# Kernel tuning notes

Hardware: AMD Instinct MI355X
Metric: run time of the kernel (lower is better)

Reference implementation:

```python
import jax, jax.numpy as jnp
import numpy as np

B, S, K, N = 4, 2048, 4096, 4096

def setup_inputs() -> dict:
    key = jax.random.key(0)
    k1, k2, k3, k4 = jax.random.split(key, 4)
    # int8 quantized activations and weight (stored as int8, matmul accumulates int32)
    a = jax.random.randint(k1, (B, S, K), -128, 128, dtype=jnp.int32).astype(jnp.int8)
    w = jax.random.randint(k3, (K, N), -128, 128, dtype=jnp.int32).astype(jnp.int8)
    # dequant scales: per-token for activations, per-output-channel for weight
    a_s = (jax.random.uniform(k2, (B, S, 1), dtype=jnp.float32) + 0.5) * 0.01
    w_s = (jax.random.uniform(k4, (1, N), dtype=jnp.float32) + 0.5) * 0.01
    return {"a": a, "a_s": a_s, "w": w, "w_s": w_s}

def reference(a, a_s, w, w_s):
    # torch._int_mm loop with padding), fused with dequant epilogue.
    acc = jnp.einsum('bsk,kn->bsn', a, w, preferred_element_type=jnp.int32)
    # dequant: float32 accum * input_scale * weight_scale, cast to model dtype (fp16)
    out = (acc.astype(jnp.float32) * a_s * w_s).astype(jnp.float16)
    return out
```

## Files before the change

### kernel.cpp

```cpp
#include <hip/hip_runtime.h>
#include <cstdint>
#include <cstddef>


#define M_DIM 8192
#define N_DIM 4096
#define K_DIM 4096

#define PACKA_BLOCKS ((M_DIM * K_DIM / 4) / 256)
#define TRANS_BLOCKS ((N_DIM / 64) * (K_DIM / 64))

typedef int v4i  __attribute__((ext_vector_type(4)));
typedef int v16i __attribute__((ext_vector_type(16)));

__device__ __forceinline__ uint32_t pack4(int x, int y, int z, int w)
{
    return (uint32_t)(x & 0xff) | ((uint32_t)(y & 0xff) << 8) |
           ((uint32_t)(z & 0xff) << 16) | ((uint32_t)(w & 0xff) << 24);
}

__global__ void __launch_bounds__(256) prepare_kernel(
    const int* __restrict__ a, const int* __restrict__ w,
    uint8_t* __restrict__ pa, uint8_t* __restrict__ wt)
{
    __shared__ int lds[64][65];

    if (blockIdx.x < PACKA_BLOCKS) {
        const size_t idx = (size_t)blockIdx.x * 256 + threadIdx.x;
        int4 x = ((const int4*)a)[idx];
        ((uint32_t*)pa)[idx] = pack4(x.x, x.y, x.z, x.w);
        return;
    }

    const int tile = blockIdx.x - PACKA_BLOCKS;
    const int t  = threadIdx.x;
    const int n0 = (tile & 63) * 64;
    const int k0 = (tile >> 6) * 64;

#pragma unroll
    for (int i = 0; i < 4; ++i) {
        int v   = t + 256 * i;
        int row = v >> 4;
        int cq  = v & 15;
        int4 x = *(const int4*)(w + (size_t)(k0 + row) * N_DIM + n0 + cq * 4);
        lds[row][cq * 4 + 0] = x.x;
        lds[row][cq * 4 + 1] = x.y;
        lds[row][cq * 4 + 2] = x.z;
        lds[row][cq * 4 + 3] = x.w;
    }
    __syncthreads();

    const int n_local = t >> 2;
    const int c       = t & 3;
    uint32_t o[4];
#pragma unroll
    for (int j = 0; j < 4; ++j)
        o[j] = pack4(lds[c * 16 + j * 4 + 0][n_local],
                     lds[c * 16 + j * 4 + 1][n_local],
                     lds[c * 16 + j * 4 + 2][n_local],
                     lds[c * 16 + j * 4 + 3][n_local]);
    *(uint4*)(wt + (size_t)(n0 + n_local) * K_DIM + k0 + c * 16) =
        make_uint4(o[0], o[1], o[2], o[3]);
}

__device__ __forceinline__ void async_copy16(const void* gptr, void* lptr)
{
    __builtin_amdgcn_global_load_lds(
        (const __attribute__((address_space(1))) uint32_t*)gptr,
        (__attribute__((address_space(3))) uint32_t*)lptr,
        16, 0, 0);
}

#define VMCNT4() asm volatile("s_waitcnt vmcnt(4)" ::: "memory")
#define VMCNT0() asm volatile("s_waitcnt vmcnt(0)" ::: "memory")

__global__ void __launch_bounds__(512, 2) int8_gemm_kernel(
    const uint8_t* __restrict__ A,
    const uint8_t* __restrict__ Wt,
    const float*   __restrict__ a_s,
    const float*   __restrict__ w_s,
    float*         __restrict__ out)
{
    __shared__ __align__(16) uint8_t sA[2][2][256 * 64];
    __shared__ __align__(16) uint8_t sB[2][2][256 * 64];

    const int tid   = threadIdx.x;
    const int wave  = tid >> 6;
    const int lane  = tid & 63;
    const int waveM = wave >> 2;
    const int waveN = wave & 3;

    const int bm = blockIdx.x & 31;
    const int bn = blockIdx.x >> 5;
    const int m0 = bm * 256;
    const int n0 = bn * 256;

    v16i acc[4][2];
#pragma unroll
    for (int i = 0; i < 4; ++i)
#pragma unroll
        for (int j = 0; j < 2; ++j)
#pragma unroll
            for (int r = 0; r < 16; ++r)
                acc[i][j][r] = 0;

    auto stageA = [&](int buf, int kh, int kt) {
#pragma unroll
        for (int l = 0; l < 2; ++l) {
            const int region = l * 8 + wave;
            const int i      = region * 64 + lane;
            const int row    = i >> 2;
            const int g      = (i & 3) ^ ((row >> 1) & 3);
            async_copy16(A + (size_t)(m0 + row) * K_DIM + kt * 128 + kh * 64 + g * 16,
                         &sA[buf][kh][region * 1024]);
        }
    };
    auto stageB = [&](int buf, int kh, int kt) {
#pragma unroll
        for (int l = 0; l < 2; ++l) {
            const int region = l * 8 + wave;
            const int i      = region * 64 + lane;
            const int row    = i >> 2;
            const int g      = (i & 3) ^ ((row >> 1) & 3);
            async_copy16(Wt + (size_t)(n0 + row) * K_DIM + kt * 128 + kh * 64 + g * 16,
                         &sB[buf][kh][region * 1024]);
        }
    };

    const int frow = lane & 31;
    const int fk   = lane >> 5;

    auto compute_kstep = [&](int buf, int s) {
        const int kh = s >> 1;
        const int c  = (s & 1) * 2 + fk;
        v4i af[4], bf[2];
#pragma unroll
        for (int mt = 0; mt < 4; ++mt) {
            const int ra = waveM * 128 + mt * 32 + frow;
            af[mt] = *(const v4i*)(&sA[buf][kh][ra * 64 + ((c ^ ((ra >> 1) & 3)) << 4)]);
        }
#pragma unroll
        for (int nt = 0; nt < 2; ++nt) {
            const int rb = waveN * 64 + nt * 32 + frow;
            bf[nt] = *(const v4i*)(&sB[buf][kh][rb * 64 + ((c ^ ((rb >> 1) & 3)) << 4)]);
        }
        __builtin_amdgcn_s_setprio(1);
#pragma unroll
        for (int mt = 0; mt < 4; ++mt)
#pragma unroll
            for (int nt = 0; nt < 2; ++nt)
                acc[mt][nt] = __builtin_amdgcn_mfma_i32_32x32x32_i8(
                    af[mt], bf[nt], acc[mt][nt], 0, 0, 0);
        __builtin_amdgcn_s_setprio(0);
    };

    const int NT = K_DIM / 128;

    stageA(0, 0, 0);
    stageB(0, 0, 0);
    stageA(0, 1, 0);
    stageB(0, 1, 0);
    VMCNT4();
    __builtin_amdgcn_s_barrier();

    for (int kt = 0; kt < NT - 1; ++kt) {
        const int b = kt & 1;
        stageA(b ^ 1, 0, kt + 1);
        compute_kstep(b, 0);
        stageB(b ^ 1, 0, kt + 1);
        compute_kstep(b, 1);
        VMCNT4();
        __builtin_amdgcn_s_barrier();
        stageA(b ^ 1, 1, kt + 1);
        compute_kstep(b, 2);
        stageB(b ^ 1, 1, kt + 1);
        compute_kstep(b, 3);
        VMCNT4();
        __builtin_amdgcn_s_barrier();
    }
    {
        const int b = (NT - 1) & 1;
        compute_kstep(b, 0);
        compute_kstep(b, 1);
        VMCNT0();
        __builtin_amdgcn_s_barrier();
        compute_kstep(b, 2);
        compute_kstep(b, 3);
    }

    const int col   = lane & 31;
    const int rbase = (lane >> 5) * 4;

#pragma unroll
    for (int mt = 0; mt < 4; ++mt) {
        const int mrow0 = m0 + waveM * 128 + mt * 32 + rbase;
        float asv[16];
#pragma unroll
        for (int reg = 0; reg < 16; ++reg)
            asv[reg] = a_s[mrow0 + (reg & 3) + 8 * (reg >> 2)];
#pragma unroll
        for (int nt = 0; nt < 2; ++nt) {
            const int n = n0 + waveN * 64 + nt * 32 + col;
            const float wsv = w_s[n];
#pragma unroll
            for (int reg = 0; reg < 16; ++reg) {
                const int row = mrow0 + (reg & 3) + 8 * (reg >> 2);
                float v = (float)acc[mt][nt][reg] * asv[reg] * wsv;
                v = (float)(_Float16)v;
                out[(size_t)row * N_DIM + n] = v;
            }
        }
    }
}

extern "C" void kernel_launch(void* const* d_in, const int* in_sizes, int n_in,
                              void* d_out, int out_size, void* d_ws, size_t ws_size,
                              hipStream_t stream)
{
    const int*   a   = (const int*)  d_in[0];
    const float* a_s = (const float*)d_in[1];
    const int*   w   = (const int*)  d_in[2];
    const float* w_s = (const float*)d_in[3];
    float*       out = (float*)d_out;

    uint8_t* wt = (uint8_t*)d_ws;
    uint8_t* pa = (uint8_t*)d_ws + (size_t)N_DIM * K_DIM;

    prepare_kernel<<<PACKA_BLOCKS + TRANS_BLOCKS, 256, 0, stream>>>(a, w, pa, wt);

    int8_gemm_kernel<<<(M_DIM / 256) * (N_DIM / 256), 512, 0, stream>>>(
        pa, wt, a_s, w_s, out);
}
```

Measured before the change: 422.3 us.

## Store LDS tiles in MFMA fragment order, simplify pipeline, remap blocks per XCD

Reorganizes shared memory so each async global-to-LDS copy lands a 32-row by 32-byte block in exact MFMA operand order. Fragment reads become linear lane*16 loads with no XOR swizzle arithmetic. The pipeline is simplified to one full-tile prefetch per iteration with a single vmcnt(0) wait and barrier, which removes the finer split overlap. Blocks are also remapped so consecutive IDs on each XCD cover 8x8 tile neighborhoods, aiming at better L2 reuse, at the risk of coarser synchronization stalls.

```diff
diff --git a/kernel.cpp b/kernel.cpp
--- a/kernel.cpp
+++ b/kernel.cpp
@@ -71,7 +71,6 @@
         16, 0, 0);
 }
 
-#define VMCNT4() asm volatile("s_waitcnt vmcnt(4)" ::: "memory")
 #define VMCNT0() asm volatile("s_waitcnt vmcnt(0)" ::: "memory")
 
 __global__ void __launch_bounds__(512, 2) int8_gemm_kernel(
@@ -81,8 +80,8 @@
     const float*   __restrict__ w_s,
     float*         __restrict__ out)
 {
-    __shared__ __align__(16) uint8_t sA[2][2][256 * 64];
-    __shared__ __align__(16) uint8_t sB[2][2][256 * 64];
+    __shared__ __align__(16) uint8_t sA[2][4][8][1024];
+    __shared__ __align__(16) uint8_t sB[2][4][8][1024];
 
     const int tid   = threadIdx.x;
     const int wave  = tid >> 6;
@@ -90,60 +89,45 @@
     const int waveM = wave >> 2;
     const int waveN = wave & 3;
 
-    const int bm = blockIdx.x & 31;
-    const int bn = blockIdx.x >> 5;
-    const int m0 = bm * 256;
-    const int n0 = bn * 256;
+    const int bid = blockIdx.x;
+    const int xc  = bid & 7;
+    const int j   = bid >> 3;
+    const int bm  = (xc & 3) * 8 + (j & 7);
+    const int bn  = (xc >> 2) * 8 + (j >> 3);
+    const int m0  = bm * 256;
+    const int n0  = bn * 256;
 
     v16i acc[4][2];
 #pragma unroll
     for (int i = 0; i < 4; ++i)
 #pragma unroll
-        for (int j = 0; j < 2; ++j)
+        for (int jj = 0; jj < 2; ++jj)
 #pragma unroll
             for (int r = 0; r < 16; ++r)
-                acc[i][j][r] = 0;
-
-    auto stageA = [&](int buf, int kh, int kt) {
-#pragma unroll
-        for (int l = 0; l < 2; ++l) {
-            const int region = l * 8 + wave;
-            const int i      = region * 64 + lane;
-            const int row    = i >> 2;
-            const int g      = (i & 3) ^ ((row >> 1) & 3);
-            async_copy16(A + (size_t)(m0 + row) * K_DIM + kt * 128 + kh * 64 + g * 16,
-                         &sA[buf][kh][region * 1024]);
+                acc[i][jj][r] = 0;
+
+    const uint8_t* aSrc = A  + (size_t)(m0 + wave * 32 + (lane & 31)) * K_DIM
+                             + ((lane >> 5) << 4);
+    const uint8_t* bSrc = Wt + (size_t)(n0 + wave * 32 + (lane & 31)) * K_DIM
+                             + ((lane >> 5) << 4);
+
+    auto stage_tile = [&](int buf, int kt) {
+        const int ko = kt * 128;
+#pragma unroll
+        for (int s = 0; s < 4; ++s) {
+            async_copy16(aSrc + ko + s * 32, &sA[buf][s][wave][0]);
+            async_copy16(bSrc + ko + s * 32, &sB[buf][s][wave][0]);
         }
     };
-    auto stageB = [&](int buf, int kh, int kt) {
-#pragma unroll
-        for (int l = 0; l < 2; ++l) {
-            const int region = l * 8 + wave;
-            const int i      = region * 64 + lane;
-            const int row    = i >> 2;
-            const int g      = (i & 3) ^ ((row >> 1) & 3);
-            async_copy16(Wt + (size_t)(n0 + row) * K_DIM + kt * 128 + kh * 64 + g * 16,
-                         &sB[buf][kh][region * 1024]);
-        }
-    };
-
-    const int frow = lane & 31;
-    const int fk   = lane >> 5;
 
     auto compute_kstep = [&](int buf, int s) {
-        const int kh = s >> 1;
-        const int c  = (s & 1) * 2 + fk;
         v4i af[4], bf[2];
 #pragma unroll
-        for (int mt = 0; mt < 4; ++mt) {
-            const int ra = waveM * 128 + mt * 32 + frow;
-            af[mt] = *(const v4i*)(&sA[buf][kh][ra * 64 + ((c ^ ((ra >> 1) & 3)) << 4)]);
-        }
-#pragma unroll
-        for (int nt = 0; nt < 2; ++nt) {
-            const int rb = waveN * 64 + nt * 32 + frow;
-            bf[nt] = *(const v4i*)(&sB[buf][kh][rb * 64 + ((c ^ ((rb >> 1) & 3)) << 4)]);
-        }
+        for (int mt = 0; mt < 4; ++mt)
+            af[mt] = *(const v4i*)(&sA[buf][s][waveM * 4 + mt][lane * 16]);
+#pragma unroll
+        for (int nt = 0; nt < 2; ++nt)
+            bf[nt] = *(const v4i*)(&sB[buf][s][waveN * 2 + nt][lane * 16]);
         __builtin_amdgcn_s_setprio(1);
 #pragma unroll
         for (int mt = 0; mt < 4; ++mt)
@@ -156,37 +140,22 @@
 
     const int NT = K_DIM / 128;
 
-    stageA(0, 0, 0);
-    stageB(0, 0, 0);
-    stageA(0, 1, 0);
-    stageB(0, 1, 0);
-    VMCNT4();
+    stage_tile(0, 0);
+    VMCNT0();
     __builtin_amdgcn_s_barrier();
 
     for (int kt = 0; kt < NT - 1; ++kt) {
         const int b = kt & 1;
-        stageA(b ^ 1, 0, kt + 1);
-        compute_kstep(b, 0);
-        stageB(b ^ 1, 0, kt + 1);
-        compute_kstep(b, 1);
-        VMCNT4();
-        __builtin_amdgcn_s_barrier();
-        stageA(b ^ 1, 1, kt + 1);
-        compute_kstep(b, 2);
-        stageB(b ^ 1, 1, kt + 1);
-        compute_kstep(b, 3);
-        VMCNT4();
-        __builtin_amdgcn_s_barrier();
-    }
-    {
-        const int b = (NT - 1) & 1;
-        compute_kstep(b, 0);
-        compute_kstep(b, 1);
+        stage_tile(b ^ 1, kt + 1);
+#pragma unroll
+        for (int s = 0; s < 4; ++s)
+            compute_kstep(b, s);
         VMCNT0();
         __builtin_amdgcn_s_barrier();
-        compute_kstep(b, 2);
-        compute_kstep(b, 3);
-    }
+    }
+#pragma unroll
+    for (int s = 0; s < 4; ++s)
+        compute_kstep((NT - 1) & 1, s);
 
     const int col   = lane & 31;
     const int rbase = (lane >> 5) * 4;
```

Result: slower. 460.5 us (+9.0%).
